# Performance work log

Hardware: AMD Instinct MI355X
Metric: run time of the kernel (lower is better)

The kernel has to match this reference:

```python
import jax, jax.numpy as jnp
import numpy as np

B, C, L = 32, 64, 4096
PS, STRIDE = 16, 8
PC = (L - PS) // STRIDE + 1  # 511
HID = 64


def setup_inputs() -> dict:
    key = jax.random.key(0)
    k = jax.random.split(key, 5)
    X = jax.random.normal(k[0], (B, C, L), dtype=jnp.float32)
    W1 = jax.random.normal(k[1], (HID, PS), dtype=jnp.float32) * 0.05  # Conv1d(1,64,PS) weight
    b1 = jax.random.normal(k[2], (HID,), dtype=jnp.float32) * 0.05
    W2 = jax.random.normal(k[3], (2, HID), dtype=jnp.float32) * 0.05   # Conv1d(64,2,1) weight
    b2 = jax.random.normal(k[4], (2,), dtype=jnp.float32) * 0.05
    return {"X": X, "W1": W1, "b1": b1, "W2": W2, "b2": b2}


def reference(X, W1, b1, W2, b2):
    Bn, Cn, Ln = X.shape
    s_bias = (PS - 1) / 2.0
    # anchors: center of each patch along the sequence axis
    anchor = jnp.arange(PC, dtype=X.dtype) * STRIDE + 0.5 * (PS - 1)  # (PC,)

    # ---- OffsetPredictor: unfold into (B, C, PC, PS) sliding windows ----
    idx = jnp.arange(PC)[:, None] * STRIDE + jnp.arange(PS)[None, :]  # (PC, PS)
    patches = X[:, :, idx]  # (B, C, PC, PS)
    # Conv1d(1, HID, PS) over a length-PS window == dense matmul with W1
    h = jax.nn.gelu(jnp.einsum('bcps,ks->bcpk', patches, W1) + b1, approximate=False)
    off = jnp.einsum('bcpk,jk->bcpj', h, W2) + b2  # (B, C, PC, 2)
    off = off.transpose(0, 2, 1, 3)  # (B, PC, C, 2)

    # ---- BoxCoder.decode ----
    dx = off[..., 0]
    ds = jax.nn.relu(off[..., 1] + s_bias)
    ref = anchor[None, :, None]
    lo = jnp.clip((dx + ref - ds) / (Ln - 1), 0.0, 1.0)  # (B, PC, C)
    hi = jnp.clip((dx + ref + ds) / (Ln - 1), 0.0, 1.0)

    # ---- BoxCoder.meshgrid: linear interp from box endpoints (align_corners) ----
    t = jnp.arange(PS, dtype=X.dtype) / (PS - 1)  # (PS,)
    xs = lo[..., None] + (hi - lo)[..., None] * t  # (B, PC, C, PS), in [0,1]
    ys = jnp.arange(Cn, dtype=X.dtype) / (Cn - 1)  # (C,), in [0,1]

    # ---- grid_sample(img=(B,1,C,L), grid=(xs,ys)*2-1, bilinear, align_corners=True) ----
    ix = xs * (Ln - 1)                                            # (B, PC, C, PS)
    iy = jnp.broadcast_to(ys[None, None, :, None] * (Cn - 1), ix.shape)
    ix0 = jnp.floor(ix)
    iy0 = jnp.floor(iy)
    wx = ix - ix0
    wy = iy - iy0
    ix0i = jnp.clip(ix0.astype(jnp.int32), 0, Ln - 1)
    ix1i = jnp.clip(ix0i + 1, 0, Ln - 1)
    iy0i = jnp.clip(iy0.astype(jnp.int32), 0, Cn - 1)
    iy1i = jnp.clip(iy0i + 1, 0, Cn - 1)

    gather = jax.vmap(lambda x, r, c: x[r, c])  # over batch; x:(C,L)
    v00 = gather(X, iy0i, ix0i)
    v01 = gather(X, iy0i, ix1i)
    v10 = gather(X, iy1i, ix0i)
    v11 = gather(X, iy1i, ix1i)
    out = (v00 * (1 - wx) + v01 * wx) * (1 - wy) + (v10 * (1 - wx) + v11 * wx) * wy
    # (B, PC, C, PS) -> (B, C, PC, PS)
    return out.transpose(0, 2, 1, 3)
```

## Files before the change

### kernel.cpp

```cpp
#include <hip/hip_runtime.h>
#include <math.h>

#define L_    4096
#define PS_   16
#define STR_  8
#define PC_   511
#define HID_  64
#define NBLK_ 2048

typedef __bf16 bf16x8 __attribute__((ext_vector_type(8)));
typedef float  f32x4  __attribute__((ext_vector_type(4)));

__device__ __forceinline__ float gelu_poly(float x) {
    float u = x * x;
    float p = fmaf(u, 4.5473e-9f,    -8.2448e-8f);
    p = fmaf(p, u,  1.33194e-6f);
    p = fmaf(p, u, -1.8889343e-5f);
    p = fmaf(p, u,  2.3087745e-4f);
    p = fmaf(p, u, -2.3746734e-3f);
    p = fmaf(p, u,  1.9947114e-2f);
    p = fmaf(p, u, -1.3298076e-1f);
    p = fmaf(p, u,  7.9788456e-1f);
    float r = x * p;
    r = fminf(fmaxf(r, -1.0f), 1.0f);
    float h = 0.5f * x;
    return fmaf(h, r, h);
}

__global__ __launch_bounds__(256) void depatch_kernel(
    const float* __restrict__ X,
    const float* __restrict__ W1,
    const float* __restrict__ b1,
    const float* __restrict__ W2,
    const float* __restrict__ b2,
    float* __restrict__ out)
{
    __shared__ __attribute__((aligned(16))) __bf16 s_rowh[L_ + 32];

    const int tid = threadIdx.x;
    const int bc  = blockIdx.x;
    const float* xrow = X + (size_t)bc * L_;

    {
        const float4* src4 = reinterpret_cast<const float4*>(xrow);
        #pragma unroll
        for (int i = 0; i < 4; ++i) {
            float4 v = src4[tid + 256 * i];
            union { __bf16 h[4]; unsigned long long u; } pk;
            pk.h[0] = (__bf16)v.x; pk.h[1] = (__bf16)v.y;
            pk.h[2] = (__bf16)v.z; pk.h[3] = (__bf16)v.w;
            *reinterpret_cast<unsigned long long*>(&s_rowh[(tid + 256 * i) * 4]) = pk.u;
        }
        if (tid < 32) s_rowh[L_ + tid] = (__bf16)0.0f;
    }

    const int l   = tid & 63;
    const int lr  = l & 15;
    const int lq  = l >> 4;
    const int lkb = lq * 8;

    bf16x8 afrag[4];
    f32x4  b1c[4];
    float  w2x[4][4], w2s[4][4];
    #pragma unroll
    for (int nb = 0; nb < 4; ++nb) {
        #pragma unroll
        for (int j = 0; j < 8; ++j) {
            int ks = lkb + j;
            afrag[nb][j] = (__bf16)((ks < PS_) ? W1[(nb * 16 + lr) * PS_ + ks] : 0.0f);
        }
        #pragma unroll
        for (int r = 0; r < 4; ++r) {
            int hid = nb * 16 + lq * 4 + r;
            b1c[nb][r] = b1[hid];
            w2x[nb][r] = W2[hid];
            w2s[nb][r] = W2[HID_ + hid];
        }
    }
    const float b20 = b2[0];
    const float b21 = b2[1];
    const float t0  = (float)lq * (4.0f / 15.0f);
    __syncthreads();

    const int wave = tid >> 6;
    float* obase = out + (size_t)bc * PC_ * PS_;

    #pragma unroll 2
    for (int gi = 0; gi < 8; ++gi) {
        const int pb = (wave * 8 + gi) * 16;
        const bf16x8 bpat = *reinterpret_cast<const bf16x8*>(&s_rowh[(pb + lr + lq) * 8]);

        f32x4 c0 = __builtin_amdgcn_mfma_f32_16x16x32_bf16(afrag[0], bpat, b1c[0], 0, 0, 0);
        f32x4 c1 = __builtin_amdgcn_mfma_f32_16x16x32_bf16(afrag[1], bpat, b1c[1], 0, 0, 0);
        f32x4 c2 = __builtin_amdgcn_mfma_f32_16x16x32_bf16(afrag[2], bpat, b1c[2], 0, 0, 0);
        f32x4 c3 = __builtin_amdgcn_mfma_f32_16x16x32_bf16(afrag[3], bpat, b1c[3], 0, 0, 0);

        float dx = 0.0f, ds = 0.0f;
#define DO_NB(cc, nb)                                        \
        {                                                    \
            _Pragma("unroll")                                \
            for (int r = 0; r < 4; ++r) {                    \
                float g = gelu_poly(cc[r]);                  \
                dx = fmaf(g, w2x[nb][r], dx);                \
                ds = fmaf(g, w2s[nb][r], ds);                \
            }                                                \
        }
        DO_NB(c0, 0) DO_NB(c1, 1) DO_NB(c2, 2) DO_NB(c3, 3)
#undef DO_NB

        dx += __shfl_xor(dx, 16, 64);  ds += __shfl_xor(ds, 16, 64);
        dx += __shfl_xor(dx, 32, 64);  ds += __shfl_xor(ds, 32, 64);
        dx += b20;  ds += b21;

        const int   p    = pb + lr;
        const float refp = (float)(p * STR_) + 7.5f;
        const float d2   = fmaxf(ds + 7.5f, 0.0f);
        const float a    = dx + refp;
        const float loi  = fminf(fmaxf(a - d2, 0.0f), 4095.0f);
        const float hii  = fminf(fmaxf(a + d2, 0.0f), 4095.0f);
        const float span = hii - loi;

        float4 o;
        float* ov = reinterpret_cast<float*>(&o);
        #pragma unroll
        for (int si = 0; si < 4; ++si) {
            float t  = t0 + (float)si * (1.0f / 15.0f);
            float ix = fmaf(span, t, loi);
            float f  = floorf(ix);
            float wx = ix - f;
            int i0 = (int)f;
            float v0 = (float)s_rowh[i0];
            float v1 = (float)s_rowh[i0 + 1];
            ov[si] = fmaf(wx, v1 - v0, v0);
        }
        if (p < PC_)
            *reinterpret_cast<float4*>(obase + (size_t)p * PS_ + lq * 4) = o;
    }
}

extern "C" void kernel_launch(void* const* d_in, const int* in_sizes, int n_in,
                              void* d_out, int out_size, void* d_ws, size_t ws_size,
                              hipStream_t stream) {
    const float* X  = (const float*)d_in[0];
    const float* W1 = (const float*)d_in[1];
    const float* b1 = (const float*)d_in[2];
    const float* W2 = (const float*)d_in[3];
    const float* b2 = (const float*)d_in[4];
    float* out = (float*)d_out;

    depatch_kernel<<<dim3(NBLK_), dim3(256), 0, stream>>>(X, W1, b1, W2, b2, out);
}
```

Measured before the change: 137.4 us.

## Use exp-based GELU, fp32 sample row, two-tile software-pipelined MFMA loop

Replaces the long polynomial erf-GELU with a sigmoid-form approximation built on hardware exp2 and reciprocal, cutting the ALU work per hidden unit. Keeps a second fp32 copy of the row in shared memory so bilinear samples read exact fp32 values instead of bf16. Restructures the loop to process two 16-patch tiles per iteration with prefetched B fragments, for more MFMA/ALU overlap, and sets launch bounds to 4 blocks per CU. The GELU approximation and the added LDS use may change accuracy and occupancy.

New measurement: 127.8 us. 7.0% less time.

```diff
diff --git a/kernel.cpp b/kernel.cpp
--- a/kernel.cpp
+++ b/kernel.cpp
@@ -11,23 +11,16 @@
 typedef __bf16 bf16x8 __attribute__((ext_vector_type(8)));
 typedef float  f32x4  __attribute__((ext_vector_type(4)));
 
-__device__ __forceinline__ float gelu_poly(float x) {
+__device__ __forceinline__ float gelu_fast(float x) {
     float u = x * x;
-    float p = fmaf(u, 4.5473e-9f,    -8.2448e-8f);
-    p = fmaf(p, u,  1.33194e-6f);
-    p = fmaf(p, u, -1.8889343e-5f);
-    p = fmaf(p, u,  2.3087745e-4f);
-    p = fmaf(p, u, -2.3746734e-3f);
-    p = fmaf(p, u,  1.9947114e-2f);
-    p = fmaf(p, u, -1.3298076e-1f);
-    p = fmaf(p, u,  7.9788456e-1f);
-    float r = x * p;
-    r = fminf(fmaxf(r, -1.0f), 1.0f);
-    float h = 0.5f * x;
-    return fmaf(h, r, h);
+    float t = fmaf(u, 0.10294294f, 2.3022082f);
+    float a = x * t;
+    float e = __builtin_amdgcn_exp2f(a);
+    float r = __builtin_amdgcn_rcpf(e + 1.0f);
+    return fmaf(-x, r, x);
 }
 
-__global__ __launch_bounds__(256) void depatch_kernel(
+__global__ __launch_bounds__(256, 4) void depatch_kernel(
     const float* __restrict__ X,
     const float* __restrict__ W1,
     const float* __restrict__ b1,
@@ -35,6 +28,7 @@
     const float* __restrict__ b2,
     float* __restrict__ out)
 {
+    __shared__ float s_row[L_ + 4];
     __shared__ __attribute__((aligned(16))) __bf16 s_rowh[L_ + 32];
 
     const int tid = threadIdx.x;
@@ -43,15 +37,18 @@
 
     {
         const float4* src4 = reinterpret_cast<const float4*>(xrow);
+        float4* dst4 = reinterpret_cast<float4*>(s_row);
         #pragma unroll
         for (int i = 0; i < 4; ++i) {
             float4 v = src4[tid + 256 * i];
+            dst4[tid + 256 * i] = v;
             union { __bf16 h[4]; unsigned long long u; } pk;
             pk.h[0] = (__bf16)v.x; pk.h[1] = (__bf16)v.y;
             pk.h[2] = (__bf16)v.z; pk.h[3] = (__bf16)v.w;
             *reinterpret_cast<unsigned long long*>(&s_rowh[(tid + 256 * i) * 4]) = pk.u;
         }
         if (tid < 32) s_rowh[L_ + tid] = (__bf16)0.0f;
+        if (tid < 4)  s_row[L_ + tid]  = 0.0f;
     }
 
     const int l   = tid & 63;
@@ -84,58 +81,86 @@
 
     const int wave = tid >> 6;
     float* obase = out + (size_t)bc * PC_ * PS_;
+    const __bf16* bbase = s_rowh + (size_t)(wave * 128 + lr + lq) * 8;
 
-    #pragma unroll 2
-    for (int gi = 0; gi < 8; ++gi) {
-        const int pb = (wave * 8 + gi) * 16;
-        const bf16x8 bpat = *reinterpret_cast<const bf16x8*>(&s_rowh[(pb + lr + lq) * 8]);
+#define MLP_REDUCE(cA0, cA1, cA2, cA3, dxv, dsv)                       \
+    {                                                                  \
+        float dx_ = 0.0f, ds_ = 0.0f;                                  \
+        _Pragma("unroll")                                              \
+        for (int r = 0; r < 4; ++r) {                                  \
+            float g0 = gelu_fast(cA0[r]);                              \
+            float g1 = gelu_fast(cA1[r]);                              \
+            float g2 = gelu_fast(cA2[r]);                              \
+            float g3 = gelu_fast(cA3[r]);                              \
+            dx_ = fmaf(g0, w2x[0][r], dx_);                            \
+            dx_ = fmaf(g1, w2x[1][r], dx_);                            \
+            dx_ = fmaf(g2, w2x[2][r], dx_);                            \
+            dx_ = fmaf(g3, w2x[3][r], dx_);                            \
+            ds_ = fmaf(g0, w2s[0][r], ds_);                            \
+            ds_ = fmaf(g1, w2s[1][r], ds_);                            \
+            ds_ = fmaf(g2, w2s[2][r], ds_);                            \
+            ds_ = fmaf(g3, w2s[3][r], ds_);                            \
+        }                                                              \
+        dx_ += __shfl_xor(dx_, 16, 64);  ds_ += __shfl_xor(ds_, 16, 64); \
+        dx_ += __shfl_xor(dx_, 32, 64);  ds_ += __shfl_xor(ds_, 32, 64); \
+        dxv = dx_ + b20;  dsv = ds_ + b21;                             \
+    }
 
-        f32x4 c0 = __builtin_amdgcn_mfma_f32_16x16x32_bf16(afrag[0], bpat, b1c[0], 0, 0, 0);
-        f32x4 c1 = __builtin_amdgcn_mfma_f32_16x16x32_bf16(afrag[1], bpat, b1c[1], 0, 0, 0);
-        f32x4 c2 = __builtin_amdgcn_mfma_f32_16x16x32_bf16(afrag[2], bpat, b1c[2], 0, 0, 0);
-        f32x4 c3 = __builtin_amdgcn_mfma_f32_16x16x32_bf16(afrag[3], bpat, b1c[3], 0, 0, 0);
+#define SAMPLE_STORE(p, dxv, dsv)                                      \
+    {                                                                  \
+        const float refp = (float)((p) * STR_) + 7.5f;                 \
+        const float d2   = fmaxf((dsv) + 7.5f, 0.0f);                  \
+        const float aa   = (dxv) + refp;                               \
+        const float loi  = fminf(fmaxf(aa - d2, 0.0f), 4095.0f);       \
+        const float hii  = fminf(fmaxf(aa + d2, 0.0f), 4095.0f);       \
+        const float span = hii - loi;                                  \
+        float4 o;                                                      \
+        float* ov = reinterpret_cast<float*>(&o);                      \
+        _Pragma("unroll")                                              \
+        for (int si = 0; si < 4; ++si) {                               \
+            float t  = t0 + (float)si * (1.0f / 15.0f);                \
+            float ix = fmaf(span, t, loi);                             \
+            float f  = floorf(ix);                                     \
+            float wx = ix - f;                                         \
+            int i0 = (int)f;                                           \
+            float v0 = s_row[i0];                                      \
+            float v1 = s_row[i0 + 1];                                  \
+            ov[si] = fmaf(wx, v1 - v0, v0);                            \
+        }                                                              \
+        if ((p) < PC_)                                                 \
+            *reinterpret_cast<float4*>(obase + (size_t)(p) * PS_ + lq * 4) = o; \
+    }
 
-        float dx = 0.0f, ds = 0.0f;
-#define DO_NB(cc, nb)                                        \
-        {                                                    \
-            _Pragma("unroll")                                \
-            for (int r = 0; r < 4; ++r) {                    \
-                float g = gelu_poly(cc[r]);                  \
-                dx = fmaf(g, w2x[nb][r], dx);                \
-                ds = fmaf(g, w2s[nb][r], ds);                \
-            }                                                \
+    bf16x8 nA = *reinterpret_cast<const bf16x8*>(bbase);
+    bf16x8 nB = *reinterpret_cast<const bf16x8*>(bbase + 128);
+
+    #pragma unroll
+    for (int i = 0; i < 4; ++i) {
+        const bf16x8 cA = nA, cB = nB;
+        if (i < 3) {
+            nA = *reinterpret_cast<const bf16x8*>(bbase + (2 * i + 2) * 128);
+            nB = *reinterpret_cast<const bf16x8*>(bbase + (2 * i + 3) * 128);
         }
-        DO_NB(c0, 0) DO_NB(c1, 1) DO_NB(c2, 2) DO_NB(c3, 3)
-#undef DO_NB
+        f32x4 a0 = __builtin_amdgcn_mfma_f32_16x16x32_bf16(afrag[0], cA, b1c[0], 0, 0, 0);
+        f32x4 a1 = __builtin_amdgcn_mfma_f32_16x16x32_bf16(afrag[1], cA, b1c[1], 0, 0, 0);
+        f32x4 a2 = __builtin_amdgcn_mfma_f32_16x16x32_bf16(afrag[2], cA, b1c[2], 0, 0, 0);
+        f32x4 a3 = __builtin_amdgcn_mfma_f32_16x16x32_bf16(afrag[3], cA, b1c[3], 0, 0, 0);
+        f32x4 q0 = __builtin_amdgcn_mfma_f32_16x16x32_bf16(afrag[0], cB, b1c[0], 0, 0, 0);
+        f32x4 q1 = __builtin_amdgcn_mfma_f32_16x16x32_bf16(afrag[1], cB, b1c[1], 0, 0, 0);
+        f32x4 q2 = __builtin_amdgcn_mfma_f32_16x16x32_bf16(afrag[2], cB, b1c[2], 0, 0, 0);
+        f32x4 q3 = __builtin_amdgcn_mfma_f32_16x16x32_bf16(afrag[3], cB, b1c[3], 0, 0, 0);
 
-        dx += __shfl_xor(dx, 16, 64);  ds += __shfl_xor(ds, 16, 64);
-        dx += __shfl_xor(dx, 32, 64);  ds += __shfl_xor(ds, 32, 64);
-        dx += b20;  ds += b21;
+        float dxA, dsA, dxB, dsB;
+        MLP_REDUCE(a0, a1, a2, a3, dxA, dsA)
+        MLP_REDUCE(q0, q1, q2, q3, dxB, dsB)
 
-        const int   p    = pb + lr;
-        const float refp = (float)(p * STR_) + 7.5f;
-        const float d2   = fmaxf(ds + 7.5f, 0.0f);
-        const float a    = dx + refp;
-        const float loi  = fminf(fmaxf(a - d2, 0.0f), 4095.0f);
-        const float hii  = fminf(fmaxf(a + d2, 0.0f), 4095.0f);
-        const float span = hii - loi;
-
-        float4 o;
-        float* ov = reinterpret_cast<float*>(&o);
-        #pragma unroll
-        for (int si = 0; si < 4; ++si) {
-            float t  = t0 + (float)si * (1.0f / 15.0f);
-            float ix = fmaf(span, t, loi);
-            float f  = floorf(ix);
-            float wx = ix - f;
-            int i0 = (int)f;
-            float v0 = (float)s_rowh[i0];
-            float v1 = (float)s_rowh[i0 + 1];
-            ov[si] = fmaf(wx, v1 - v0, v0);
-        }
-        if (p < PC_)
-            *reinterpret_cast<float4*>(obase + (size_t)p * PS_ + lq * 4) = o;
+        const int pA = wave * 128 + (2 * i) * 16 + lr;
+        const int pB = pA + 16;
+        SAMPLE_STORE(pA, dxA, dsA)
+        SAMPLE_STORE(pB, dxB, dsB)
     }
+#undef MLP_REDUCE
+#undef SAMPLE_STORE
 }
 
 extern "C" void kernel_launch(void* const* d_in, const int* in_sizes, int n_in,
```
